# Kernel optimization log

Measured on AMD Instinct MI355X. Metric: run time of the kernel, lower is better.

## Reference

```python
import jax, jax.numpy as jnp
import numpy as np

NHEADS = 16
NGROUPS = 16
NEG = -1e9

def _apply_rope(t, cos, sin):
    # t: (B,T,H,hs) -> pairs (B,T,H,hs//2,2); complex multiply by (cos + i*sin)
    B, T, H, hs = t.shape
    tp = t.reshape(B, T, H, hs // 2, 2)
    a, b = tp[..., 0], tp[..., 1]
    c = cos[None, :, None, :]
    s = sin[None, :, None, :]
    out = jnp.stack([a * c - b * s, a * s + b * c], axis=-1)
    return out.reshape(B, T, H, hs)

def _causal_attn(q, k, v):
    # q,k: (..., S, d); v: (..., S, dv); causal softmax attention, scale 1/sqrt(d)
    d = q.shape[-1]
    S = q.shape[-2]
    scores = jnp.einsum('...qd,...kd->...qk', q, k) / jnp.sqrt(jnp.asarray(d, q.dtype))
    mask = jnp.tril(jnp.ones((S, S), dtype=bool))
    scores = jnp.where(mask, scores, NEG)
    p = jax.nn.softmax(scores, axis=-1)
    return jnp.einsum('...qk,...kd->...qd', p, v)

def setup_inputs() -> dict:
    key = jax.random.key(0)
    k1, k2, k3 = jax.random.split(key, 3)
    B, T, C = 4, 2048, 1024
    hs = C // NHEADS
    x = jax.random.normal(k1, (B, T, C), dtype=jnp.float32)
    w_attn = jax.random.normal(k2, (3 * C, C), dtype=jnp.float32) * (1.0 / np.sqrt(C))
    w_proj = jax.random.normal(k3, (C, C), dtype=jnp.float32) * (1.0 / np.sqrt(C))
    # standard RoPE frequencies: theta_i = 10000^{-2i/hs}
    inv = 1.0 / (10000.0 ** (np.arange(0, hs, 2, dtype=np.float32) / hs))  # (hs//2,)
    ang = np.arange(T, dtype=np.float32)[:, None] * inv[None, :]           # (T, hs//2)
    freqs_cos = jnp.asarray(np.cos(ang), dtype=jnp.float32)
    freqs_sin = jnp.asarray(np.sin(ang), dtype=jnp.float32)
    return {'x': x, 'w_attn': w_attn, 'w_proj': w_proj,
            'freqs_cos': freqs_cos, 'freqs_sin': freqs_sin}

def reference(x, w_attn, w_proj, freqs_cos, freqs_sin):
    B, T, C = x.shape
    H = NHEADS
    hs = C // H
    G = min(T // (T // NGROUPS), NGROUPS)  # group_t = block_size // ngroups, T == block_size
    Tg = T // G
    qkv = x @ w_attn.T                      # (B,T,3C)
    q, k, v = jnp.split(qkv, 3, axis=2)
    # RoPE
    q = _apply_rope(q.reshape(B, T, H, hs), freqs_cos, freqs_sin).reshape(B, T, C)
    k = _apply_rope(k.reshape(B, T, H, hs), freqs_cos, freqs_sin).reshape(B, T, C)
    # group: (B, G, Tg, H, hs) -> (B, H, G, Tg, hs)
    def grp(t):
        return t.reshape(B, G, Tg, H, hs).transpose(0, 3, 1, 2, 4)
    q, k, v = grp(q), grp(k), grp(v)
    # its_time branch: append mean-pooled summary token per group
    q = jnp.concatenate([q, q.mean(axis=3, keepdims=True)], axis=3)  # (B,H,G,Tg+1,hs)
    k = jnp.concatenate([k, k.mean(axis=3, keepdims=True)], axis=3)
    v = jnp.concatenate([v, v.mean(axis=3, keepdims=True)], axis=3)
    att = _causal_attn(q, k, v)             # (B,H,G,Tg+1,hs)
    # group-level attention over summary tokens of all but last group
    q2 = q[:, :, :-1, -1]                   # (B,H,G-1,hs)
    k2 = k[:, :, :-1, -1]
    av = att[:, :, :-1, -1]                 # (B,H,G-1,hs)
    v2 = _causal_attn(q2, k2, av)           # (B,H,G-1,hs)
    y_q = q2[:, :, :, None, :]              # (B,H,G-1,1,hs)
    y_k = k2[:, :, :, None, :]
    y_v = v2[:, :, :, None, :]
    # drop summary tokens, merge groups back: (B,H,G,Tg,hs) -> (B,T,C)
    xo = att[:, :, :, :-1]
    xo = xo.reshape(B, H, T, hs).transpose(0, 2, 1, 3).reshape(B, T, C)
    out = xo @ w_proj.T
    return (out, y_q, y_k, y_v)
```

## Files before the change

### kernel.cpp

```cpp
#include <hip/hip_runtime.h>
#include <hip/hip_bf16.h>

#define HS 64
#define NH 16
#define NG 16
#define TT 2048
#define CC 1024
#define BBATCH 4
#define TG 128
#define SS 129

typedef __attribute__((ext_vector_type(8))) short bf16x8;
typedef __attribute__((ext_vector_type(4))) float f32x4;

__device__ __forceinline__ float bf2f(ushort u) {
  return __uint_as_float(((unsigned)u) << 16);
}
__device__ __forceinline__ ushort f2bf(float f) {
  unsigned x = __float_as_uint(f);
  x += 0x7fff + ((x >> 16) & 1);
  return (ushort)(x >> 16);
}
__device__ __forceinline__ bf16x8 mk8(ushort4 a0, ushort4 a1) {
  bf16x8 v;
  v[0] = (short)a0.x; v[1] = (short)a0.y; v[2] = (short)a0.z; v[3] = (short)a0.w;
  v[4] = (short)a1.x; v[5] = (short)a1.y; v[6] = (short)a1.z; v[7] = (short)a1.w;
  return v;
}

__global__ void cvt_f32_bf16(const float* __restrict__ src, ushort* __restrict__ dst, int n4) {
  int stride = gridDim.x * blockDim.x;
  for (int i = blockIdx.x * blockDim.x + threadIdx.x; i < n4; i += stride) {
    float4 v = ((const float4*)src)[i];
    ushort4 o;
    o.x = f2bf(v.x); o.y = f2bf(v.y); o.z = f2bf(v.z); o.w = f2bf(v.w);
    ((ushort4*)dst)[i] = o;
  }
}

template <bool OUT_BF16>
__global__ __launch_bounds__(256) void gemm_bt(const ushort* __restrict__ A,
                                               const ushort* __restrict__ Bw,
                                               void* __restrict__ Cout,
                                               int M, int N, int K) {
  __shared__ ushort As[128][68];
  __shared__ ushort Bs[128][68];
  const int m0 = blockIdx.y * 128;
  const int n0 = blockIdx.x * 128;
  const int tid = threadIdx.x;
  const int lane = tid & 63;
  const int wv = tid >> 6;
  const int wr = wv >> 1, wc = wv & 1;
  const int lo = lane & 15, hi = lane >> 4;

  f32x4 acc[4][4];
#pragma unroll
  for (int i = 0; i < 4; ++i)
#pragma unroll
    for (int j = 0; j < 4; ++j) acc[i][j] = (f32x4)0.0f;

  for (int k0 = 0; k0 < K; k0 += 64) {
    __syncthreads();
#pragma unroll
    for (int t = 0; t < 4; ++t) {
      int c = tid + 256 * t;
      int row = c >> 3, cc = c & 7;
      uint4 va = *(const uint4*)(A + (size_t)(m0 + row) * K + k0 + cc * 8);
      *(uint2*)&As[row][cc * 8]     = make_uint2(va.x, va.y);
      *(uint2*)&As[row][cc * 8 + 4] = make_uint2(va.z, va.w);
      uint4 vb = *(const uint4*)(Bw + (size_t)(n0 + row) * K + k0 + cc * 8);
      *(uint2*)&Bs[row][cc * 8]     = make_uint2(vb.x, vb.y);
      *(uint2*)&Bs[row][cc * 8 + 4] = make_uint2(vb.z, vb.w);
    }
    __syncthreads();
#pragma unroll
    for (int kk = 0; kk < 64; kk += 32) {
      bf16x8 af[4], bfr[4];
#pragma unroll
      for (int i = 0; i < 4; ++i) {
        int r = wr * 64 + i * 16 + lo;
        af[i] = mk8(*(const ushort4*)&As[r][kk + 4 * hi],
                    *(const ushort4*)&As[r][kk + 16 + 4 * hi]);
      }
#pragma unroll
      for (int j = 0; j < 4; ++j) {
        int r = wc * 64 + j * 16 + lo;
        bfr[j] = mk8(*(const ushort4*)&Bs[r][kk + 4 * hi],
                     *(const ushort4*)&Bs[r][kk + 16 + 4 * hi]);
      }
#pragma unroll
      for (int i = 0; i < 4; ++i)
#pragma unroll
        for (int j = 0; j < 4; ++j)
          acc[i][j] = __builtin_amdgcn_mfma_f32_16x16x32_bf16(af[i], bfr[j], acc[i][j], 0, 0, 0);
    }
  }
#pragma unroll
  for (int i = 0; i < 4; ++i) {
    int row = m0 + wr * 64 + i * 16 + 4 * hi;
#pragma unroll
    for (int j = 0; j < 4; ++j) {
      int col = n0 + wc * 64 + j * 16 + lo;
#pragma unroll
      for (int r = 0; r < 4; ++r) {
        float v = acc[i][j][r];
        if constexpr (OUT_BF16) {
          ((ushort*)Cout)[(size_t)(row + r) * N + col] = f2bf(v);
        } else {
          ((float*)Cout)[(size_t)(row + r) * N + col] = v;
        }
      }
    }
  }
}

__global__ __launch_bounds__(256) void rope_group(const ushort* __restrict__ qkv,
                                                  const float* __restrict__ fc,
                                                  const float* __restrict__ fs,
                                                  ushort* __restrict__ qg, ushort* __restrict__ kg,
                                                  ushort* __restrict__ vg,
                                                  float* __restrict__ yq, float* __restrict__ yk) {
  int blk = blockIdx.x;
  int g = blk & 15, h = (blk >> 4) & 15, b = blk >> 8;
  int tid = threadIdx.x;
  int d2 = tid & 31, s0 = tid >> 5;
  size_t gbase = (size_t)blk * SS * HS;
  float sq0 = 0, sq1 = 0, sk0 = 0, sk1 = 0, sv0 = 0, sv1 = 0;
#pragma unroll
  for (int it = 0; it < 16; ++it) {
    int s = s0 + 8 * it;
    int t = g * TG + s;
    size_t rowoff = ((size_t)(b * TT + t)) * (3 * CC) + h * HS + 2 * d2;
    float c = fc[t * 32 + d2], sn = fs[t * 32 + d2];
    ushort2 qu = *(const ushort2*)(qkv + rowoff);
    float qa = bf2f(qu.x), qb = bf2f(qu.y);
    float rq0 = qa * c - qb * sn, rq1 = qa * sn + qb * c;
    ushort2 ku = *(const ushort2*)(qkv + rowoff + CC);
    float ka = bf2f(ku.x), kb = bf2f(ku.y);
    float rk0 = ka * c - kb * sn, rk1 = ka * sn + kb * c;
    ushort2 vu = *(const ushort2*)(qkv + rowoff + 2 * CC);
    float v0 = bf2f(vu.x), v1 = bf2f(vu.y);
    *(ushort2*)(qg + gbase + s * HS + 2 * d2) = make_ushort2(f2bf(rq0), f2bf(rq1));
    *(ushort2*)(kg + gbase + s * HS + 2 * d2) = make_ushort2(f2bf(rk0), f2bf(rk1));
    *(ushort2*)(vg + gbase + s * HS + 2 * d2) = vu;
    sq0 += rq0; sq1 += rq1; sk0 += rk0; sk1 += rk1; sv0 += v0; sv1 += v1;
  }
  __shared__ float red[256][6];
  red[tid][0] = sq0; red[tid][1] = sq1; red[tid][2] = sk0;
  red[tid][3] = sk1; red[tid][4] = sv0; red[tid][5] = sv1;
  __syncthreads();
  if (tid < 32) {
    float m[6];
#pragma unroll
    for (int c = 0; c < 6; ++c) {
      float acc = 0;
#pragma unroll
      for (int r = 0; r < 8; ++r) acc += red[r * 32 + tid][c];
      m[c] = acc * (1.0f / 128.0f);
    }
    *(ushort2*)(qg + gbase + 128 * HS + 2 * tid) = make_ushort2(f2bf(m[0]), f2bf(m[1]));
    *(ushort2*)(kg + gbase + 128 * HS + 2 * tid) = make_ushort2(f2bf(m[2]), f2bf(m[3]));
    *(ushort2*)(vg + gbase + 128 * HS + 2 * tid) = make_ushort2(f2bf(m[4]), f2bf(m[5]));
    if (g < 15) {
      size_t yo = ((size_t)(b * 16 + h) * 15 + g) * 64 + 2 * tid;
      yq[yo] = m[0]; yq[yo + 1] = m[1];
      yk[yo] = m[2]; yk[yo + 1] = m[3];
    }
  }
}

__global__ __launch_bounds__(256) void attn1(const ushort* __restrict__ qg,
                                             const ushort* __restrict__ kg,
                                             const ushort* __restrict__ vg,
                                             ushort* __restrict__ xo, float* __restrict__ attm) {
  __shared__ ushort qs[144][68];
  __shared__ ushort ks[144][68];
  __shared__ ushort vt[64][148];
  __shared__ ushort obuf[4][16][68];
  const int blk = blockIdx.x;
  const int g = blk & 15, h = (blk >> 4) & 15, b = blk >> 8;
  const int tid = threadIdx.x;
  const int lane = tid & 63, wv = tid >> 6;
  const int lo = lane & 15, hi = lane >> 4;
  const size_t gbase = (size_t)blk * SS * HS;

  {
    ushort* vflat = &vt[0][0];
    for (int idx = tid; idx < 64 * 148 / 4; idx += 256)
      *(ushort4*)(vflat + idx * 4) = make_ushort4(0, 0, 0, 0);
  }
  __syncthreads();
  for (int idx = tid; idx < 144 * 16; idx += 256) {
    int s = idx >> 4, c = (idx & 15) * 4;
    if (s < SS) {
      *(ushort4*)&qs[s][c] = *(const ushort4*)(qg + gbase + s * HS + c);
      *(ushort4*)&ks[s][c] = *(const ushort4*)(kg + gbase + s * HS + c);
      ushort4 v4 = *(const ushort4*)(vg + gbase + s * HS + c);
      vt[c][s] = v4.x; vt[c + 1][s] = v4.y; vt[c + 2][s] = v4.z; vt[c + 3][s] = v4.w;
    } else {
      *(ushort4*)&qs[s][c] = make_ushort4(0, 0, 0, 0);
      *(ushort4*)&ks[s][c] = make_ushort4(0, 0, 0, 0);
    }
  }
  __syncthreads();

#pragma unroll
  for (int ti = 0; ti < 3; ++ti) {
    const int t = (ti == 0) ? (8 - wv)
                : (ti == 1) ? ((wv == 3) ? 4 : (wv + 1))
                            : ((wv == 3) ? 0 : -1);
    if (t < 0) continue;
    const int q0 = t * 16;

    bf16x8 bq[2];
#pragma unroll
    for (int k2 = 0; k2 < 2; ++k2)
      bq[k2] = mk8(*(const ushort4*)&qs[q0 + lo][k2 * 32 + 4 * hi],
                   *(const ushort4*)&qs[q0 + lo][k2 * 32 + 16 + 4 * hi]);

    f32x4 sc[9];
#pragma unroll
    for (int n = 0; n < 9; ++n) sc[n] = (f32x4)0.0f;
#pragma unroll
    for (int n = 0; n < 9; ++n) {
      if (n > t) continue;
#pragma unroll
      for (int k2 = 0; k2 < 2; ++k2) {
        bf16x8 ak = mk8(*(const ushort4*)&ks[n * 16 + lo][k2 * 32 + 4 * hi],
                        *(const ushort4*)&ks[n * 16 + lo][k2 * 32 + 16 + 4 * hi]);
        sc[n] = __builtin_amdgcn_mfma_f32_16x16x32_bf16(ak, bq[k2], sc[n], 0, 0, 0);
      }
    }

    const int qi = q0 + lo;
    float mx = -INFINITY;
#pragma unroll
    for (int n = 0; n < 9; ++n) {
      if (n > t) continue;
#pragma unroll
      for (int r = 0; r < 4; ++r) {
        int kj = n * 16 + 4 * hi + r;
        float v = (kj <= qi) ? sc[n][r] * 0.125f : -INFINITY;
        sc[n][r] = v;
        mx = fmaxf(mx, v);
      }
    }
    mx = fmaxf(mx, __shfl_xor(mx, 16));
    mx = fmaxf(mx, __shfl_xor(mx, 32));
    float sum = 0.f;
#pragma unroll
    for (int n = 0; n < 9; ++n) {
      if (n > t) continue;
#pragma unroll
      for (int r = 0; r < 4; ++r) {
        float e = __expf(sc[n][r] - mx);
        sc[n][r] = e;
        sum += e;
      }
    }
    sum += __shfl_xor(sum, 16);
    sum += __shfl_xor(sum, 32);
    const float inv = 1.0f / sum;

    f32x4 oac[4];
#pragma unroll
    for (int m = 0; m < 4; ++m) oac[m] = (f32x4)0.0f;
#pragma unroll
    for (int s2 = 0; s2 < 5; ++s2) {
      if (s2 > (t >> 1)) continue;
      const int kt1ok = (2 * s2 + 1 <= t);
      bf16x8 pb;
#pragma unroll
      for (int e = 0; e < 4; ++e) pb[e] = (short)f2bf(sc[2 * s2][e] * inv);
      if (kt1ok) {
#pragma unroll
        for (int e = 0; e < 4; ++e) pb[e + 4] = (short)f2bf(sc[2 * s2 + 1][e] * inv);
      } else {
#pragma unroll
        for (int e = 0; e < 4; ++e) pb[e + 4] = 0;
      }
#pragma unroll
      for (int m = 0; m < 4; ++m) {
        ushort4 a0 = *(const ushort4*)&vt[m * 16 + lo][32 * s2 + 4 * hi];
        ushort4 a1 = kt1ok ? *(const ushort4*)&vt[m * 16 + lo][32 * s2 + 16 + 4 * hi]
                           : make_ushort4(0, 0, 0, 0);
        oac[m] = __builtin_amdgcn_mfma_f32_16x16x32_bf16(mk8(a0, a1), pb, oac[m], 0, 0, 0);
      }
    }

    if (t < 8) {
#pragma unroll
      for (int m = 0; m < 4; ++m)
#pragma unroll
        for (int r = 0; r < 4; ++r)
          obuf[wv][lo][m * 16 + 4 * hi + r] = f2bf(oac[m][r]);
#pragma unroll
      for (int it = 0; it < 4; ++it) {
        int idx = lane + 64 * it;
        int r = idx >> 4;
        int c4 = (idx & 15) * 4;
        uint2 val = *(const uint2*)&obuf[wv][r][c4];
        int tok = g * TG + t * 16 + r;
        *(uint2*)(xo + ((size_t)(b * TT + tok)) * CC + h * HS + c4) = val;
      }
    } else {
      if (lo == 0) {
#pragma unroll
        for (int m = 0; m < 4; ++m)
#pragma unroll
          for (int r = 0; r < 4; ++r)
            attm[(size_t)blk * 64 + m * 16 + 4 * hi + r] = oac[m][r];
      }
    }
  }
}

__global__ __launch_bounds__(64) void attn2(const float* __restrict__ yq,
                                            const float* __restrict__ yk,
                                            const float* __restrict__ attm,
                                            float* __restrict__ yv) {
  __shared__ float qs2[15][64], ks2[15][64], avs[15][64], srow[16];
  int bh = blockIdx.x, lane = threadIdx.x;
  for (int j = 0; j < 15; ++j) {
    qs2[j][lane] = yq[((size_t)bh * 15 + j) * 64 + lane];
    ks2[j][lane] = yk[((size_t)bh * 15 + j) * 64 + lane];
    avs[j][lane] = attm[((size_t)bh * 16 + j) * 64 + lane];
  }
  __syncthreads();
  for (int i = 0; i < 15; ++i) {
    float qv = qs2[i][lane];
    for (int j = 0; j <= i; ++j) {
      float t = qv * ks2[j][lane];
#pragma unroll
      for (int off = 32; off > 0; off >>= 1) t += __shfl_xor(t, off);
      if (lane == 0) srow[j] = t * 0.125f;
    }
    __syncthreads();
    float mx = -INFINITY;
    for (int j = 0; j <= i; ++j) mx = fmaxf(mx, srow[j]);
    float den = 0;
    for (int j = 0; j <= i; ++j) den += __expf(srow[j] - mx);
    float inv = 1.0f / den;
    float o = 0;
    for (int j = 0; j <= i; ++j) o += __expf(srow[j] - mx) * inv * avs[j][lane];
    yv[((size_t)bh * 15 + i) * 64 + lane] = o;
    __syncthreads();
  }
}

extern "C" void kernel_launch(void* const* d_in, const int* in_sizes, int n_in,
                              void* d_out, int out_size, void* d_ws, size_t ws_size,
                              hipStream_t stream) {
  const float* x      = (const float*)d_in[0];
  const float* w_attn = (const float*)d_in[1];
  const float* w_proj = (const float*)d_in[2];
  const float* fc     = (const float*)d_in[3];
  const float* fs     = (const float*)d_in[4];
  float* out = (float*)d_out;

  char* ws = (char*)d_ws;
  ushort* xb   = (ushort*)(ws);
  ushort* xo   = (ushort*)(ws);
  ushort* wab  = (ushort*)(ws + 16777216);
  float*  attm = (float*) (ws + 16777216);
  ushort* wpb  = (ushort*)(ws + 23068672);
  ushort* qkv  = (ushort*)(ws + 25165824);
  ushort* qg   = (ushort*)(ws + 75497472);
  ushort* kg   = (ushort*)(ws + 92405760);
  ushort* vg   = (ushort*)(ws + 109314048);

  float* yq = out + 8388608;
  float* yk = out + 8450048;
  float* yv = out + 8511488;

  cvt_f32_bf16<<<2048, 256, 0, stream>>>(x, xb, 8388608 / 4);
  cvt_f32_bf16<<<1024, 256, 0, stream>>>(w_attn, wab, 3145728 / 4);
  cvt_f32_bf16<<<512, 256, 0, stream>>>(w_proj, wpb, 1048576 / 4);
  gemm_bt<true><<<dim3(24, 64), 256, 0, stream>>>(xb, wab, qkv, 8192, 3072, 1024);
  rope_group<<<1024, 256, 0, stream>>>(qkv, fc, fs, qg, kg, vg, yq, yk);
  attn1<<<1024, 256, 0, stream>>>(qg, kg, vg, xo, attm);
  attn2<<<64, 64, 0, stream>>>(yq, yk, attm, yv);
  gemm_bt<false><<<dim3(8, 64), 256, 0, stream>>>(xo, wpb, out, 8192, 1024, 1024);
}
```

Baseline: 199.4 us.

## Fuse RoPE, grouping and mean pooling into QKV GEMM epilogue with direct LDS loads

Removes the separate rope_group kernel and the bf16 qkv intermediate. The QKV GEMM epilogue now applies RoPE to q and k, using lane shuffles to pair adjacent columns. It scatters results straight into the grouped q/k/v layout and computes per-group column means through a shared-memory reduction. Both GEMMs also switch to global_load_lds 16-byte direct-to-LDS loads with an unpadded 64-wide tile, which replaces the register round trip. The trade-offs are scattered 2-byte epilogue stores, per-element cos/sin loads, and possible LDS bank conflicts from the unpadded layout.

```diff
diff --git a/kernel.cpp b/kernel.cpp
--- a/kernel.cpp
+++ b/kernel.cpp
@@ -27,6 +27,10 @@
   v[4] = (short)a1.x; v[5] = (short)a1.y; v[6] = (short)a1.z; v[7] = (short)a1.w;
   return v;
 }
+__device__ __forceinline__ void load_lds16(const ushort* g, ushort* l) {
+  __builtin_amdgcn_global_load_lds((const __attribute__((address_space(1))) unsigned int*)g,
+                                   (__attribute__((address_space(3))) unsigned int*)l, 16, 0, 0);
+}
 
 __global__ void cvt_f32_bf16(const float* __restrict__ src, ushort* __restrict__ dst, int n4) {
   int stride = gridDim.x * blockDim.x;
@@ -38,13 +42,44 @@
   }
 }
 
+#define GEMM_CORE(A_, B_, K_, m0_, n0_)                                            \
+  {                                                                                \
+    const int rA = tid >> 3, cA = (tid & 7) * 8;                                   \
+    for (int k0 = 0; k0 < (K_); k0 += 64) {                                        \
+      _Pragma("unroll")                                                            \
+      for (int it = 0; it < 4; ++it) {                                             \
+        load_lds16((A_) + (size_t)((m0_) + it * 32 + rA) * (K_) + k0 + cA,         \
+                   As + it * 2048 + wv * 512);                                     \
+        load_lds16((B_) + (size_t)((n0_) + it * 32 + rA) * (K_) + k0 + cA,         \
+                   Bs + it * 2048 + wv * 512);                                     \
+      }                                                                            \
+      __syncthreads();                                                             \
+      _Pragma("unroll")                                                            \
+      for (int kk = 0; kk < 64; kk += 32) {                                        \
+        bf16x8 af[4], bfr[4];                                                      \
+        _Pragma("unroll")                                                          \
+        for (int i = 0; i < 4; ++i)                                                \
+          af[i] = *(const bf16x8*)(As + (wr * 64 + i * 16 + lo) * 64 + kk + 8 * hi); \
+        _Pragma("unroll")                                                          \
+        for (int j = 0; j < 4; ++j)                                                \
+          bfr[j] = *(const bf16x8*)(Bs + (wc * 64 + j * 16 + lo) * 64 + kk + 8 * hi); \
+        _Pragma("unroll")                                                          \
+        for (int i = 0; i < 4; ++i)                                                \
+          _Pragma("unroll")                                                        \
+          for (int j = 0; j < 4; ++j)                                              \
+            acc[i][j] = __builtin_amdgcn_mfma_f32_16x16x32_bf16(af[i], bfr[j], acc[i][j], 0, 0, 0); \
+      }                                                                            \
+      __syncthreads();                                                             \
+    }                                                                              \
+  }
+
 template <bool OUT_BF16>
 __global__ __launch_bounds__(256) void gemm_bt(const ushort* __restrict__ A,
                                                const ushort* __restrict__ Bw,
                                                void* __restrict__ Cout,
                                                int M, int N, int K) {
-  __shared__ ushort As[128][68];
-  __shared__ ushort Bs[128][68];
+  __shared__ ushort As[128 * 64];
+  __shared__ ushort Bs[128 * 64];
   const int m0 = blockIdx.y * 128;
   const int n0 = blockIdx.x * 128;
   const int tid = threadIdx.x;
@@ -59,42 +94,8 @@
 #pragma unroll
     for (int j = 0; j < 4; ++j) acc[i][j] = (f32x4)0.0f;
 
-  for (int k0 = 0; k0 < K; k0 += 64) {
-    __syncthreads();
-#pragma unroll
-    for (int t = 0; t < 4; ++t) {
-      int c = tid + 256 * t;
-      int row = c >> 3, cc = c & 7;
-      uint4 va = *(const uint4*)(A + (size_t)(m0 + row) * K + k0 + cc * 8);
-      *(uint2*)&As[row][cc * 8]     = make_uint2(va.x, va.y);
-      *(uint2*)&As[row][cc * 8 + 4] = make_uint2(va.z, va.w);
-      uint4 vb = *(const uint4*)(Bw + (size_t)(n0 + row) * K + k0 + cc * 8);
-      *(uint2*)&Bs[row][cc * 8]     = make_uint2(vb.x, vb.y);
-      *(uint2*)&Bs[row][cc * 8 + 4] = make_uint2(vb.z, vb.w);
-    }
-    __syncthreads();
-#pragma unroll
-    for (int kk = 0; kk < 64; kk += 32) {
-      bf16x8 af[4], bfr[4];
-#pragma unroll
-      for (int i = 0; i < 4; ++i) {
-        int r = wr * 64 + i * 16 + lo;
-        af[i] = mk8(*(const ushort4*)&As[r][kk + 4 * hi],
-                    *(const ushort4*)&As[r][kk + 16 + 4 * hi]);
-      }
-#pragma unroll
-      for (int j = 0; j < 4; ++j) {
-        int r = wc * 64 + j * 16 + lo;
-        bfr[j] = mk8(*(const ushort4*)&Bs[r][kk + 4 * hi],
-                     *(const ushort4*)&Bs[r][kk + 16 + 4 * hi]);
-      }
-#pragma unroll
-      for (int i = 0; i < 4; ++i)
-#pragma unroll
-        for (int j = 0; j < 4; ++j)
-          acc[i][j] = __builtin_amdgcn_mfma_f32_16x16x32_bf16(af[i], bfr[j], acc[i][j], 0, 0, 0);
-    }
-  }
+  GEMM_CORE(A, Bw, K, m0, n0)
+
 #pragma unroll
   for (int i = 0; i < 4; ++i) {
     int row = m0 + wr * 64 + i * 16 + 4 * hi;
@@ -114,57 +115,92 @@
   }
 }
 
-__global__ __launch_bounds__(256) void rope_group(const ushort* __restrict__ qkv,
-                                                  const float* __restrict__ fc,
-                                                  const float* __restrict__ fs,
-                                                  ushort* __restrict__ qg, ushort* __restrict__ kg,
-                                                  ushort* __restrict__ vg,
-                                                  float* __restrict__ yq, float* __restrict__ yk) {
-  int blk = blockIdx.x;
-  int g = blk & 15, h = (blk >> 4) & 15, b = blk >> 8;
-  int tid = threadIdx.x;
-  int d2 = tid & 31, s0 = tid >> 5;
-  size_t gbase = (size_t)blk * SS * HS;
-  float sq0 = 0, sq1 = 0, sk0 = 0, sk1 = 0, sv0 = 0, sv1 = 0;
-#pragma unroll
-  for (int it = 0; it < 16; ++it) {
-    int s = s0 + 8 * it;
-    int t = g * TG + s;
-    size_t rowoff = ((size_t)(b * TT + t)) * (3 * CC) + h * HS + 2 * d2;
-    float c = fc[t * 32 + d2], sn = fs[t * 32 + d2];
-    ushort2 qu = *(const ushort2*)(qkv + rowoff);
-    float qa = bf2f(qu.x), qb = bf2f(qu.y);
-    float rq0 = qa * c - qb * sn, rq1 = qa * sn + qb * c;
-    ushort2 ku = *(const ushort2*)(qkv + rowoff + CC);
-    float ka = bf2f(ku.x), kb = bf2f(ku.y);
-    float rk0 = ka * c - kb * sn, rk1 = ka * sn + kb * c;
-    ushort2 vu = *(const ushort2*)(qkv + rowoff + 2 * CC);
-    float v0 = bf2f(vu.x), v1 = bf2f(vu.y);
-    *(ushort2*)(qg + gbase + s * HS + 2 * d2) = make_ushort2(f2bf(rq0), f2bf(rq1));
-    *(ushort2*)(kg + gbase + s * HS + 2 * d2) = make_ushort2(f2bf(rk0), f2bf(rk1));
-    *(ushort2*)(vg + gbase + s * HS + 2 * d2) = vu;
-    sq0 += rq0; sq1 += rq1; sk0 += rk0; sk1 += rk1; sv0 += v0; sv1 += v1;
-  }
-  __shared__ float red[256][6];
-  red[tid][0] = sq0; red[tid][1] = sq1; red[tid][2] = sk0;
-  red[tid][3] = sk1; red[tid][4] = sv0; red[tid][5] = sv1;
+__global__ __launch_bounds__(256) void gemm_qkv_rope(const ushort* __restrict__ A,
+                                                     const ushort* __restrict__ Bw,
+                                                     const float* __restrict__ fc,
+                                                     const float* __restrict__ fs,
+                                                     ushort* __restrict__ qg,
+                                                     ushort* __restrict__ kg,
+                                                     ushort* __restrict__ vg,
+                                                     float* __restrict__ yq,
+                                                     float* __restrict__ yk) {
+  __shared__ ushort As[128 * 64];
+  __shared__ ushort Bs[128 * 64];
+  __shared__ float colsum[2][128];
+  const int K = CC, m0 = blockIdx.y * 128, n0 = blockIdx.x * 128;
+  const int tid = threadIdx.x;
+  const int lane = tid & 63;
+  const int wv = tid >> 6;
+  const int wr = wv >> 1, wc = wv & 1;
+  const int lo = lane & 15, hi = lane >> 4;
+
+  f32x4 acc[4][4];
+#pragma unroll
+  for (int i = 0; i < 4; ++i)
+#pragma unroll
+    for (int j = 0; j < 4; ++j) acc[i][j] = (f32x4)0.0f;
+
+  GEMM_CORE(A, Bw, K, m0, n0)
+
+  const int b = m0 >> 11;
+  const int tseq0 = m0 & 2047;
+  const int g = tseq0 >> 7;
+  const int part = n0 >> 10;
+  const int cbase = n0 & 1023;
+  ushort* G = part == 0 ? qg : (part == 1 ? kg : vg);
+
+  float msum[4] = {0.f, 0.f, 0.f, 0.f};
+#pragma unroll
+  for (int j = 0; j < 4; ++j) {
+    const int col = wc * 64 + j * 16 + lo;
+    const int d = (cbase + col) & 63;
+    const int h = (cbase + col) >> 6;
+    const int blk = (b * 16 + h) * 16 + g;
+    ushort* dst = G + ((size_t)blk * SS) * 64 + d;
+#pragma unroll
+    for (int i = 0; i < 4; ++i) {
+#pragma unroll
+      for (int r = 0; r < 4; ++r) {
+        const int row = wr * 64 + i * 16 + 4 * hi + r;
+        float v = acc[i][j][r];
+        float o;
+        if (part < 2) {
+          float p = __shfl_xor(v, 1);
+          const int ts = tseq0 + row;
+          float cc2 = fc[ts * 32 + (d >> 1)];
+          float sn2 = fs[ts * 32 + (d >> 1)];
+          o = (d & 1) ? (p * sn2 + v * cc2) : (v * cc2 - p * sn2);
+        } else {
+          o = v;
+        }
+        msum[j] += o;
+        dst[(size_t)row * 64] = f2bf(o);
+      }
+    }
+  }
+#pragma unroll
+  for (int j = 0; j < 4; ++j) {
+    msum[j] += __shfl_xor(msum[j], 16);
+    msum[j] += __shfl_xor(msum[j], 32);
+  }
+  if (hi == 0) {
+#pragma unroll
+    for (int j = 0; j < 4; ++j) colsum[wr][wc * 64 + j * 16 + lo] = msum[j];
+  }
   __syncthreads();
-  if (tid < 32) {
-    float m[6];
-#pragma unroll
-    for (int c = 0; c < 6; ++c) {
-      float acc = 0;
-#pragma unroll
-      for (int r = 0; r < 8; ++r) acc += red[r * 32 + tid][c];
-      m[c] = acc * (1.0f / 128.0f);
-    }
-    *(ushort2*)(qg + gbase + 128 * HS + 2 * tid) = make_ushort2(f2bf(m[0]), f2bf(m[1]));
-    *(ushort2*)(kg + gbase + 128 * HS + 2 * tid) = make_ushort2(f2bf(m[2]), f2bf(m[3]));
-    *(ushort2*)(vg + gbase + 128 * HS + 2 * tid) = make_ushort2(f2bf(m[4]), f2bf(m[5]));
-    if (g < 15) {
-      size_t yo = ((size_t)(b * 16 + h) * 15 + g) * 64 + 2 * tid;
-      yq[yo] = m[0]; yq[yo + 1] = m[1];
-      yk[yo] = m[2]; yk[yo + 1] = m[3];
+  if (wr == 0 && hi == 0) {
+#pragma unroll
+    for (int j = 0; j < 4; ++j) {
+      const int col = wc * 64 + j * 16 + lo;
+      const float mean = (colsum[0][col] + colsum[1][col]) * (1.0f / 128.0f);
+      const int d = (cbase + col) & 63;
+      const int h = (cbase + col) >> 6;
+      const int blk = (b * 16 + h) * 16 + g;
+      G[((size_t)blk * SS + 128) * 64 + d] = f2bf(mean);
+      if (g < 15 && part < 2) {
+        float* Y = (part == 0) ? yq : yk;
+        Y[((size_t)(b * 16 + h) * 15 + g) * 64 + d] = mean;
+      }
     }
   }
 }
@@ -364,10 +400,9 @@
   ushort* wab  = (ushort*)(ws + 16777216);
   float*  attm = (float*) (ws + 16777216);
   ushort* wpb  = (ushort*)(ws + 23068672);
-  ushort* qkv  = (ushort*)(ws + 25165824);
-  ushort* qg   = (ushort*)(ws + 75497472);
-  ushort* kg   = (ushort*)(ws + 92405760);
-  ushort* vg   = (ushort*)(ws + 109314048);
+  ushort* qg   = (ushort*)(ws + 25165824);
+  ushort* kg   = (ushort*)(ws + 42074112);
+  ushort* vg   = (ushort*)(ws + 58982400);
 
   float* yq = out + 8388608;
   float* yk = out + 8450048;
@@ -376,8 +411,7 @@
   cvt_f32_bf16<<<2048, 256, 0, stream>>>(x, xb, 8388608 / 4);
   cvt_f32_bf16<<<1024, 256, 0, stream>>>(w_attn, wab, 3145728 / 4);
   cvt_f32_bf16<<<512, 256, 0, stream>>>(w_proj, wpb, 1048576 / 4);
-  gemm_bt<true><<<dim3(24, 64), 256, 0, stream>>>(xb, wab, qkv, 8192, 3072, 1024);
-  rope_group<<<1024, 256, 0, stream>>>(qkv, fc, fs, qg, kg, vg, yq, yk);
+  gemm_qkv_rope<<<dim3(24, 64), 256, 0, stream>>>(xb, wab, fc, fs, qg, kg, vg, yq, yk);
   attn1<<<1024, 256, 0, stream>>>(qg, kg, vg, xo, attm);
   attn2<<<64, 64, 0, stream>>>(yq, yk, attm, yv);
   gemm_bt<false><<<dim3(8, 64), 256, 0, stream>>>(xo, wpb, out, 8192, 1024, 1024);
```

Result: slower. 227.4 us (+14.0%).

## Rewrite GEMM with direct-to-LDS async loads, multi-buffering and swizzled tiles

Applied to the files above, without the earlier changes.

Replaces the simple 128x128 GEMM with a 256x128-tile, 512-thread kernel. It stages A and B straight into LDS through global_load_lds, double-buffers A and triple-buffers B, uses an XOR swizzle on the LDS layout, raises MFMA priority with setprio, and remaps block IDs for L2 locality. The aim is to overlap global loads with MFMA work and cut LDS bank conflicts and register staging. Attn1 also now reads Q fragments straight from global memory instead of LDS and zero-fills only the padding of the V tile, which lowers LDS use and setup work. The hand-placed waitcnt and barrier logic is fragile if any of the counts are wrong.

```diff
diff --git a/kernel.cpp b/kernel.cpp
--- a/kernel.cpp
+++ b/kernel.cpp
@@ -27,6 +27,10 @@
   v[4] = (short)a1.x; v[5] = (short)a1.y; v[6] = (short)a1.z; v[7] = (short)a1.w;
   return v;
 }
+__device__ __forceinline__ void load_lds16(const ushort* g, ushort* l) {
+  __builtin_amdgcn_global_load_lds((const __attribute__((address_space(1))) unsigned int*)g,
+                                   (__attribute__((address_space(3))) unsigned int*)l, 16, 0, 0);
+}
 
 __global__ void cvt_f32_bf16(const float* __restrict__ src, ushort* __restrict__ dst, int n4) {
   int stride = gridDim.x * blockDim.x;
@@ -39,19 +43,28 @@
 }
 
 template <bool OUT_BF16>
-__global__ __launch_bounds__(256) void gemm_bt(const ushort* __restrict__ A,
-                                               const ushort* __restrict__ Bw,
-                                               void* __restrict__ Cout,
-                                               int M, int N, int K) {
-  __shared__ ushort As[128][68];
-  __shared__ ushort Bs[128][68];
-  const int m0 = blockIdx.y * 128;
-  const int n0 = blockIdx.x * 128;
+__global__ __launch_bounds__(512, 2) void gemm8p(const ushort* __restrict__ A,
+                                                 const ushort* __restrict__ Bw,
+                                                 void* __restrict__ Cout,
+                                                 int N, int K, int nx) {
+  __shared__ ushort Ab[2 * 256 * 64];
+  __shared__ ushort Bb[3 * 128 * 64];
   const int tid = threadIdx.x;
-  const int lane = tid & 63;
-  const int wv = tid >> 6;
-  const int wr = wv >> 1, wc = wv & 1;
-  const int lo = lane & 15, hi = lane >> 4;
+  const int w = tid >> 6, lane = tid & 63;
+  const int lo = lane & 15, hi4 = lane >> 4;
+  const int wm = w >> 1, wn = w & 1;
+  const int nwg = gridDim.x;
+  const int cpx = nwg >> 3;
+  const int bid = blockIdx.x;
+  const int swz = (bid & 7) * cpx + (bid >> 3);
+  const int n0 = (swz % nx) * 128;
+  const int m0 = (swz / nx) * 256;
+  const int srow = lane >> 3;
+  const int scol = ((lane & 7) * 8) ^ (srow << 3);
+  const int nt = K >> 6;
+
+  const ushort* Ag = A + (size_t)(m0 + w * 8 + srow) * K + scol;
+  const ushort* Bg = Bw + (size_t)(n0 + w * 8 + srow) * K + scol;
 
   f32x4 acc[4][4];
 #pragma unroll
@@ -59,55 +72,136 @@
 #pragma unroll
     for (int j = 0; j < 4; ++j) acc[i][j] = (f32x4)0.0f;
 
-  for (int k0 = 0; k0 < K; k0 += 64) {
-    __syncthreads();
-#pragma unroll
-    for (int t = 0; t < 4; ++t) {
-      int c = tid + 256 * t;
-      int row = c >> 3, cc = c & 7;
-      uint4 va = *(const uint4*)(A + (size_t)(m0 + row) * K + k0 + cc * 8);
-      *(uint2*)&As[row][cc * 8]     = make_uint2(va.x, va.y);
-      *(uint2*)&As[row][cc * 8 + 4] = make_uint2(va.z, va.w);
-      uint4 vb = *(const uint4*)(Bw + (size_t)(n0 + row) * K + k0 + cc * 8);
-      *(uint2*)&Bs[row][cc * 8]     = make_uint2(vb.x, vb.y);
-      *(uint2*)&Bs[row][cc * 8 + 4] = make_uint2(vb.z, vb.w);
-    }
-    __syncthreads();
-#pragma unroll
-    for (int kk = 0; kk < 64; kk += 32) {
-      bf16x8 af[4], bfr[4];
-#pragma unroll
-      for (int i = 0; i < 4; ++i) {
-        int r = wr * 64 + i * 16 + lo;
-        af[i] = mk8(*(const ushort4*)&As[r][kk + 4 * hi],
-                    *(const ushort4*)&As[r][kk + 16 + 4 * hi]);
-      }
-#pragma unroll
-      for (int j = 0; j < 4; ++j) {
-        int r = wc * 64 + j * 16 + lo;
-        bfr[j] = mk8(*(const ushort4*)&Bs[r][kk + 4 * hi],
-                     *(const ushort4*)&Bs[r][kk + 16 + 4 * hi]);
-      }
-#pragma unroll
-      for (int i = 0; i < 4; ++i)
-#pragma unroll
-        for (int j = 0; j < 4; ++j)
-          acc[i][j] = __builtin_amdgcn_mfma_f32_16x16x32_bf16(af[i], bfr[j], acc[i][j], 0, 0, 0);
-    }
-  }
+  const int cx = (lane & 7) << 3;
+  const int c0 = (8 * hi4) ^ cx;
+  const int c1 = (32 + 8 * hi4) ^ cx;
+  const int rowA = (wm * 64 + lo) * 64;
+  const int rowB = (wn * 64 + lo) * 64;
+
+#define STG_A2(tt, ab, p0)                                                          \
+  {                                                                                 \
+    load_lds16(Ag + (size_t)((p0) * 64) * K + (tt) * 64,                            \
+               Ab + (ab) * 16384 + (p0) * 4096 + w * 512);                          \
+    load_lds16(Ag + (size_t)((p0) * 64 + 64) * K + (tt) * 64,                       \
+               Ab + (ab) * 16384 + ((p0) + 1) * 4096 + w * 512);                    \
+  }
+#define STG_B(tt, bb)                                                               \
+  {                                                                                 \
+    load_lds16(Bg + (tt) * 64, Bb + (bb) * 8192 + w * 512);                         \
+    load_lds16(Bg + (size_t)64 * K + (tt) * 64, Bb + (bb) * 8192 + 4096 + w * 512); \
+  }
+
+  STG_A2(0, 0, 0)
+  STG_A2(0, 0, 2)
+  STG_B(0, 0)
+  STG_B(1, 1)
+  asm volatile("s_waitcnt vmcnt(2)" ::: "memory");
+  __builtin_amdgcn_s_barrier();
+  __builtin_amdgcn_sched_barrier(0);
+
+  int acur = 0, bcur = 0, bs1 = 1, bs2 = 2;
+  for (int t = 0; t < nt; ++t) {
+    if (t > 0) {
+      if (t < nt - 1) {
+        asm volatile("s_waitcnt vmcnt(2)" ::: "memory");
+      } else {
+        asm volatile("s_waitcnt vmcnt(0)" ::: "memory");
+      }
+      __builtin_amdgcn_s_barrier();
+      __builtin_amdgcn_sched_barrier(0);
+    }
+    const ushort* Ac = Ab + acur * 16384;
+    const ushort* Bc = Bb + bcur * 8192;
+    const int an = acur ^ 1;
+    const bool pfA = (t + 1) < nt;
+    const bool pfB = (t + 2) < nt;
+    bf16x8 bfrag[4][2];
+    bf16x8 a0, a1;
+
+    if (pfA) STG_A2(t + 1, an, 0)
+#pragma unroll
+    for (int j = 0; j < 4; ++j) {
+      bfrag[j][0] = *(const bf16x8*)(Bc + rowB + j * 1024 + c0);
+      bfrag[j][1] = *(const bf16x8*)(Bc + rowB + j * 1024 + c1);
+    }
+    a0 = *(const bf16x8*)(Ac + rowA + c0);
+    a1 = *(const bf16x8*)(Ac + rowA + c1);
+    asm volatile("s_waitcnt lgkmcnt(0)" ::: "memory");
+    __builtin_amdgcn_sched_barrier(0);
+    __builtin_amdgcn_s_setprio(1);
+#pragma unroll
+    for (int j = 0; j < 4; ++j) {
+      acc[0][j] = __builtin_amdgcn_mfma_f32_16x16x32_bf16(a0, bfrag[j][0], acc[0][j], 0, 0, 0);
+      acc[0][j] = __builtin_amdgcn_mfma_f32_16x16x32_bf16(a1, bfrag[j][1], acc[0][j], 0, 0, 0);
+    }
+    __builtin_amdgcn_s_setprio(0);
+    __builtin_amdgcn_s_barrier();
+    __builtin_amdgcn_sched_barrier(0);
+
+    if (pfA) STG_A2(t + 1, an, 2)
+    a0 = *(const bf16x8*)(Ac + 1024 + rowA + c0);
+    a1 = *(const bf16x8*)(Ac + 1024 + rowA + c1);
+    asm volatile("s_waitcnt lgkmcnt(0)" ::: "memory");
+    __builtin_amdgcn_sched_barrier(0);
+    __builtin_amdgcn_s_setprio(1);
+#pragma unroll
+    for (int j = 0; j < 4; ++j) {
+      acc[1][j] = __builtin_amdgcn_mfma_f32_16x16x32_bf16(a0, bfrag[j][0], acc[1][j], 0, 0, 0);
+      acc[1][j] = __builtin_amdgcn_mfma_f32_16x16x32_bf16(a1, bfrag[j][1], acc[1][j], 0, 0, 0);
+    }
+    __builtin_amdgcn_s_setprio(0);
+    __builtin_amdgcn_s_barrier();
+    __builtin_amdgcn_sched_barrier(0);
+
+    if (pfB) STG_B(t + 2, bs2)
+    a0 = *(const bf16x8*)(Ac + 2048 + rowA + c0);
+    a1 = *(const bf16x8*)(Ac + 2048 + rowA + c1);
+    asm volatile("s_waitcnt lgkmcnt(0)" ::: "memory");
+    __builtin_amdgcn_sched_barrier(0);
+    __builtin_amdgcn_s_setprio(1);
+#pragma unroll
+    for (int j = 0; j < 4; ++j) {
+      acc[2][j] = __builtin_amdgcn_mfma_f32_16x16x32_bf16(a0, bfrag[j][0], acc[2][j], 0, 0, 0);
+      acc[2][j] = __builtin_amdgcn_mfma_f32_16x16x32_bf16(a1, bfrag[j][1], acc[2][j], 0, 0, 0);
+    }
+    __builtin_amdgcn_s_setprio(0);
+    __builtin_amdgcn_s_barrier();
+    __builtin_amdgcn_sched_barrier(0);
+
+    a0 = *(const bf16x8*)(Ac + 3072 + rowA + c0);
+    a1 = *(const bf16x8*)(Ac + 3072 + rowA + c1);
+    asm volatile("s_waitcnt lgkmcnt(0)" ::: "memory");
+    __builtin_amdgcn_sched_barrier(0);
+    __builtin_amdgcn_s_setprio(1);
+#pragma unroll
+    for (int j = 0; j < 4; ++j) {
+      acc[3][j] = __builtin_amdgcn_mfma_f32_16x16x32_bf16(a0, bfrag[j][0], acc[3][j], 0, 0, 0);
+      acc[3][j] = __builtin_amdgcn_mfma_f32_16x16x32_bf16(a1, bfrag[j][1], acc[3][j], 0, 0, 0);
+    }
+    __builtin_amdgcn_s_setprio(0);
+    __builtin_amdgcn_s_barrier();
+    __builtin_amdgcn_sched_barrier(0);
+
+    acur ^= 1;
+    int tmp = bcur; bcur = bs1; bs1 = bs2; bs2 = tmp;
+  }
+#undef STG_A2
+#undef STG_B
+
+  const int crow = m0 + wm * 64 + 4 * hi4;
+  const int ccol = n0 + wn * 64 + lo;
 #pragma unroll
   for (int i = 0; i < 4; ++i) {
-    int row = m0 + wr * 64 + i * 16 + 4 * hi;
-#pragma unroll
-    for (int j = 0; j < 4; ++j) {
-      int col = n0 + wc * 64 + j * 16 + lo;
+#pragma unroll
+    for (int j = 0; j < 4; ++j) {
 #pragma unroll
       for (int r = 0; r < 4; ++r) {
-        float v = acc[i][j][r];
+        const int row = crow + i * 16 + r;
+        const int col = ccol + j * 16;
         if constexpr (OUT_BF16) {
-          ((ushort*)Cout)[(size_t)(row + r) * N + col] = f2bf(v);
+          ((ushort*)Cout)[(size_t)row * N + col] = f2bf(acc[i][j][r]);
         } else {
-          ((float*)Cout)[(size_t)(row + r) * N + col] = v;
+          ((float*)Cout)[(size_t)row * N + col] = acc[i][j][r];
         }
       }
     }
@@ -173,7 +267,6 @@
                                              const ushort* __restrict__ kg,
                                              const ushort* __restrict__ vg,
                                              ushort* __restrict__ xo, float* __restrict__ attm) {
-  __shared__ ushort qs[144][68];
   __shared__ ushort ks[144][68];
   __shared__ ushort vt[64][148];
   __shared__ ushort obuf[4][16][68];
@@ -184,23 +277,16 @@
   const int lo = lane & 15, hi = lane >> 4;
   const size_t gbase = (size_t)blk * SS * HS;
 
-  {
-    ushort* vflat = &vt[0][0];
-    for (int idx = tid; idx < 64 * 148 / 4; idx += 256)
-      *(ushort4*)(vflat + idx * 4) = make_ushort4(0, 0, 0, 0);
+  for (int idx = tid; idx < 320; idx += 256) {
+    int d = idx / 5, ch = (idx % 5) * 4;
+    *(ushort4*)&vt[d][128 + ch] = make_ushort4(0, 0, 0, 0);
   }
   __syncthreads();
-  for (int idx = tid; idx < 144 * 16; idx += 256) {
+  for (int idx = tid; idx < SS * 16; idx += 256) {
     int s = idx >> 4, c = (idx & 15) * 4;
-    if (s < SS) {
-      *(ushort4*)&qs[s][c] = *(const ushort4*)(qg + gbase + s * HS + c);
-      *(ushort4*)&ks[s][c] = *(const ushort4*)(kg + gbase + s * HS + c);
-      ushort4 v4 = *(const ushort4*)(vg + gbase + s * HS + c);
-      vt[c][s] = v4.x; vt[c + 1][s] = v4.y; vt[c + 2][s] = v4.z; vt[c + 3][s] = v4.w;
-    } else {
-      *(ushort4*)&qs[s][c] = make_ushort4(0, 0, 0, 0);
-      *(ushort4*)&ks[s][c] = make_ushort4(0, 0, 0, 0);
-    }
+    *(ushort4*)&ks[s][c] = *(const ushort4*)(kg + gbase + s * HS + c);
+    ushort4 v4 = *(const ushort4*)(vg + gbase + s * HS + c);
+    vt[c][s] = v4.x; vt[c + 1][s] = v4.y; vt[c + 2][s] = v4.z; vt[c + 3][s] = v4.w;
   }
   __syncthreads();
 
@@ -212,11 +298,12 @@
     if (t < 0) continue;
     const int q0 = t * 16;
 
+    const ushort* qrow = qg + gbase + (size_t)(q0 + lo) * HS;
     bf16x8 bq[2];
 #pragma unroll
     for (int k2 = 0; k2 < 2; ++k2)
-      bq[k2] = mk8(*(const ushort4*)&qs[q0 + lo][k2 * 32 + 4 * hi],
-                   *(const ushort4*)&qs[q0 + lo][k2 * 32 + 16 + 4 * hi]);
+      bq[k2] = mk8(*(const ushort4*)(qrow + k2 * 32 + 4 * hi),
+                   *(const ushort4*)(qrow + k2 * 32 + 16 + 4 * hi));
 
     f32x4 sc[9];
 #pragma unroll
@@ -376,9 +463,9 @@
   cvt_f32_bf16<<<2048, 256, 0, stream>>>(x, xb, 8388608 / 4);
   cvt_f32_bf16<<<1024, 256, 0, stream>>>(w_attn, wab, 3145728 / 4);
   cvt_f32_bf16<<<512, 256, 0, stream>>>(w_proj, wpb, 1048576 / 4);
-  gemm_bt<true><<<dim3(24, 64), 256, 0, stream>>>(xb, wab, qkv, 8192, 3072, 1024);
+  gemm8p<true><<<768, 512, 0, stream>>>(xb, wab, qkv, 3072, 1024, 24);
   rope_group<<<1024, 256, 0, stream>>>(qkv, fc, fs, qg, kg, vg, yq, yk);
   attn1<<<1024, 256, 0, stream>>>(qg, kg, vg, xo, attm);
   attn2<<<64, 64, 0, stream>>>(yq, yk, attm, yv);
-  gemm_bt<false><<<dim3(8, 64), 256, 0, stream>>>(xo, wpb, out, 8192, 1024, 1024);
-}
+  gemm8p<false><<<256, 512, 0, stream>>>(xo, wpb, out, 1024, 1024, 8);
+}
```

After: 221.3 us. 1.11x slower.

## Stage GEMM tiles with direct global-to-LDS loads and swizzle block order

Applied to the files above, without the earlier changes.

The GEMM now fills its shared-memory tiles with global_load_lds 16-byte loads that go straight into an unpadded 64-wide LDS layout. Fragments are read as single 8-element vectors, and the block index is remapped across 8 chunks to improve cache locality. The attention kernel drops its Q shared-memory staging and reads Q fragments straight from global memory, and it only zero-fills the padding columns of the transposed V tile. The risks are LDS bank conflicts from the unpadded 128-byte row stride, and Q/K padding rows that now hold uninitialised or neighbouring-group data instead of zeros.

```diff
diff --git a/kernel.cpp b/kernel.cpp
--- a/kernel.cpp
+++ b/kernel.cpp
@@ -27,6 +27,10 @@
   v[4] = (short)a1.x; v[5] = (short)a1.y; v[6] = (short)a1.z; v[7] = (short)a1.w;
   return v;
 }
+__device__ __forceinline__ void load_lds16(const ushort* g, ushort* l) {
+  __builtin_amdgcn_global_load_lds((const __attribute__((address_space(1))) unsigned int*)g,
+                                   (__attribute__((address_space(3))) unsigned int*)l, 16, 0, 0);
+}
 
 __global__ void cvt_f32_bf16(const float* __restrict__ src, ushort* __restrict__ dst, int n4) {
   int stride = gridDim.x * blockDim.x;
@@ -38,15 +42,49 @@
   }
 }
 
+#define GEMM_CORE(A_, B_, K_, m0_, n0_)                                            \
+  {                                                                                \
+    const int rA = tid >> 3, cA = (tid & 7) * 8;                                   \
+    for (int k0 = 0; k0 < (K_); k0 += 64) {                                        \
+      _Pragma("unroll")                                                            \
+      for (int it = 0; it < 4; ++it) {                                             \
+        load_lds16((A_) + (size_t)((m0_) + it * 32 + rA) * (K_) + k0 + cA,         \
+                   As + it * 2048 + wv * 512);                                     \
+        load_lds16((B_) + (size_t)((n0_) + it * 32 + rA) * (K_) + k0 + cA,         \
+                   Bs + it * 2048 + wv * 512);                                     \
+      }                                                                            \
+      __syncthreads();                                                             \
+      _Pragma("unroll")                                                            \
+      for (int kk = 0; kk < 64; kk += 32) {                                        \
+        bf16x8 af[4], bfr[4];                                                      \
+        _Pragma("unroll")                                                          \
+        for (int i = 0; i < 4; ++i)                                                \
+          af[i] = *(const bf16x8*)(As + (wr * 64 + i * 16 + lo) * 64 + kk + 8 * hi); \
+        _Pragma("unroll")                                                          \
+        for (int j = 0; j < 4; ++j)                                                \
+          bfr[j] = *(const bf16x8*)(Bs + (wc * 64 + j * 16 + lo) * 64 + kk + 8 * hi); \
+        _Pragma("unroll")                                                          \
+        for (int i = 0; i < 4; ++i)                                                \
+          _Pragma("unroll")                                                        \
+          for (int j = 0; j < 4; ++j)                                              \
+            acc[i][j] = __builtin_amdgcn_mfma_f32_16x16x32_bf16(af[i], bfr[j], acc[i][j], 0, 0, 0); \
+      }                                                                            \
+      __syncthreads();                                                             \
+    }                                                                              \
+  }
+
 template <bool OUT_BF16>
 __global__ __launch_bounds__(256) void gemm_bt(const ushort* __restrict__ A,
                                                const ushort* __restrict__ Bw,
                                                void* __restrict__ Cout,
                                                int M, int N, int K) {
-  __shared__ ushort As[128][68];
-  __shared__ ushort Bs[128][68];
-  const int m0 = blockIdx.y * 128;
-  const int n0 = blockIdx.x * 128;
+  __shared__ ushort As[128 * 64];
+  __shared__ ushort Bs[128 * 64];
+  const int id = blockIdx.x + gridDim.x * blockIdx.y;
+  const int chunk = (gridDim.x * gridDim.y) >> 3;
+  const int nid = (id & 7) * chunk + (id >> 3);
+  const int m0 = (nid / gridDim.x) * 128;
+  const int n0 = (nid % gridDim.x) * 128;
   const int tid = threadIdx.x;
   const int lane = tid & 63;
   const int wv = tid >> 6;
@@ -59,42 +97,8 @@
 #pragma unroll
     for (int j = 0; j < 4; ++j) acc[i][j] = (f32x4)0.0f;
 
-  for (int k0 = 0; k0 < K; k0 += 64) {
-    __syncthreads();
-#pragma unroll
-    for (int t = 0; t < 4; ++t) {
-      int c = tid + 256 * t;
-      int row = c >> 3, cc = c & 7;
-      uint4 va = *(const uint4*)(A + (size_t)(m0 + row) * K + k0 + cc * 8);
-      *(uint2*)&As[row][cc * 8]     = make_uint2(va.x, va.y);
-      *(uint2*)&As[row][cc * 8 + 4] = make_uint2(va.z, va.w);
-      uint4 vb = *(const uint4*)(Bw + (size_t)(n0 + row) * K + k0 + cc * 8);
-      *(uint2*)&Bs[row][cc * 8]     = make_uint2(vb.x, vb.y);
-      *(uint2*)&Bs[row][cc * 8 + 4] = make_uint2(vb.z, vb.w);
-    }
-    __syncthreads();
-#pragma unroll
-    for (int kk = 0; kk < 64; kk += 32) {
-      bf16x8 af[4], bfr[4];
-#pragma unroll
-      for (int i = 0; i < 4; ++i) {
-        int r = wr * 64 + i * 16 + lo;
-        af[i] = mk8(*(const ushort4*)&As[r][kk + 4 * hi],
-                    *(const ushort4*)&As[r][kk + 16 + 4 * hi]);
-      }
-#pragma unroll
-      for (int j = 0; j < 4; ++j) {
-        int r = wc * 64 + j * 16 + lo;
-        bfr[j] = mk8(*(const ushort4*)&Bs[r][kk + 4 * hi],
-                     *(const ushort4*)&Bs[r][kk + 16 + 4 * hi]);
-      }
-#pragma unroll
-      for (int i = 0; i < 4; ++i)
-#pragma unroll
-        for (int j = 0; j < 4; ++j)
-          acc[i][j] = __builtin_amdgcn_mfma_f32_16x16x32_bf16(af[i], bfr[j], acc[i][j], 0, 0, 0);
-    }
-  }
+  GEMM_CORE(A, Bw, K, m0, n0)
+
 #pragma unroll
   for (int i = 0; i < 4; ++i) {
     int row = m0 + wr * 64 + i * 16 + 4 * hi;
@@ -173,7 +177,6 @@
                                              const ushort* __restrict__ kg,
                                              const ushort* __restrict__ vg,
                                              ushort* __restrict__ xo, float* __restrict__ attm) {
-  __shared__ ushort qs[144][68];
   __shared__ ushort ks[144][68];
   __shared__ ushort vt[64][148];
   __shared__ ushort obuf[4][16][68];
@@ -184,23 +187,16 @@
   const int lo = lane & 15, hi = lane >> 4;
   const size_t gbase = (size_t)blk * SS * HS;
 
-  {
-    ushort* vflat = &vt[0][0];
-    for (int idx = tid; idx < 64 * 148 / 4; idx += 256)
-      *(ushort4*)(vflat + idx * 4) = make_ushort4(0, 0, 0, 0);
+  for (int idx = tid; idx < 320; idx += 256) {
+    int d = idx / 5, ch = (idx % 5) * 4;
+    *(ushort4*)&vt[d][128 + ch] = make_ushort4(0, 0, 0, 0);
   }
   __syncthreads();
-  for (int idx = tid; idx < 144 * 16; idx += 256) {
+  for (int idx = tid; idx < SS * 16; idx += 256) {
     int s = idx >> 4, c = (idx & 15) * 4;
-    if (s < SS) {
-      *(ushort4*)&qs[s][c] = *(const ushort4*)(qg + gbase + s * HS + c);
-      *(ushort4*)&ks[s][c] = *(const ushort4*)(kg + gbase + s * HS + c);
-      ushort4 v4 = *(const ushort4*)(vg + gbase + s * HS + c);
-      vt[c][s] = v4.x; vt[c + 1][s] = v4.y; vt[c + 2][s] = v4.z; vt[c + 3][s] = v4.w;
-    } else {
-      *(ushort4*)&qs[s][c] = make_ushort4(0, 0, 0, 0);
-      *(ushort4*)&ks[s][c] = make_ushort4(0, 0, 0, 0);
-    }
+    *(ushort4*)&ks[s][c] = *(const ushort4*)(kg + gbase + s * HS + c);
+    ushort4 v4 = *(const ushort4*)(vg + gbase + s * HS + c);
+    vt[c][s] = v4.x; vt[c + 1][s] = v4.y; vt[c + 2][s] = v4.z; vt[c + 3][s] = v4.w;
   }
   __syncthreads();
 
@@ -212,11 +208,12 @@
     if (t < 0) continue;
     const int q0 = t * 16;
 
+    const ushort* qrow = qg + gbase + (size_t)(q0 + lo) * HS;
     bf16x8 bq[2];
 #pragma unroll
     for (int k2 = 0; k2 < 2; ++k2)
-      bq[k2] = mk8(*(const ushort4*)&qs[q0 + lo][k2 * 32 + 4 * hi],
-                   *(const ushort4*)&qs[q0 + lo][k2 * 32 + 16 + 4 * hi]);
+      bq[k2] = mk8(*(const ushort4*)(qrow + k2 * 32 + 4 * hi),
+                   *(const ushort4*)(qrow + k2 * 32 + 16 + 4 * hi));
 
     f32x4 sc[9];
 #pragma unroll
```

Result: slower. 210.3 us (+5.4%).
